# Kernel tuning notes

Measured on AMD Instinct MI355X. Metric: run time of the kernel, lower is better.

Reference implementation:

```python
import jax, jax.numpy as jnp
import numpy as np

N, E, IN, C, ED = 100000, 1600000, 128, 64, 16
L, SC, NCL, NM = 3, 256, 2, 4000  # n_conv_layers, classifier width, n_classifier_layers, n_graphs
INV_SQRT_C = 1.0 / np.sqrt(C).astype(np.float32)


def _w(k, shape):
    fan_in = shape[-2] if len(shape) > 1 else shape[-1]
    return jax.random.normal(k, shape, jnp.float32) / np.sqrt(fan_in).astype(np.float32)


def setup_inputs() -> dict:
    key = jax.random.key(0)
    ks = jax.random.split(key, 40)
    inp = {
        "x": jax.random.normal(ks[0], (N, IN), jnp.float32),
        "edge_index": jax.random.randint(ks[1], (2, E), 0, N, jnp.int32),
        "edge_attr": jax.random.normal(ks[2], (E, ED), jnp.float32),
        "batch": jnp.sort(jax.random.randint(ks[3], (N,), 0, NM, jnp.int32)),
        # conv1 (IN -> C), heads=1
        "Wq1": _w(ks[4], (IN, C)), "bq1": jnp.zeros((C,), jnp.float32),
        "Wk1": _w(ks[5], (IN, C)), "bk1": jnp.zeros((C,), jnp.float32),
        "Wv1": _w(ks[6], (IN, C)), "bv1": jnp.zeros((C,), jnp.float32),
        "We1": _w(ks[7], (ED, C)),  # lin_edge has no bias in PyG TransformerConv
        "Ws1": _w(ks[8], (IN, C)), "bs1": jnp.zeros((C,), jnp.float32),
        # stacked conv layers (C -> C)
        "Wq": _w(ks[9], (L, C, C)), "bq": jnp.zeros((L, C), jnp.float32),
        "Wk": _w(ks[10], (L, C, C)), "bk": jnp.zeros((L, C), jnp.float32),
        "Wv": _w(ks[11], (L, C, C)), "bv": jnp.zeros((L, C), jnp.float32),
        "We": _w(ks[12], (L, ED, C)),
        "Ws": _w(ks[13], (L, C, C)), "bs": jnp.zeros((L, C), jnp.float32),
        # classifier head
        "W1": _w(ks[14], (C * (L + 1), SC)), "b1": jnp.zeros((SC,), jnp.float32),
        "Wc": _w(ks[15], (NCL, SC, SC)), "bc": jnp.zeros((NCL, SC), jnp.float32),
        "Wf": _w(ks[16], (SC, 1)), "bf": jnp.zeros((1,), jnp.float32),
    }
    return inp


def _tconv(h, src, dst, ea_proj_in, Wq, bq, Wk, bk, Wv, bv, We, Ws, bs):
    n = h.shape[0]
    q = h @ Wq + bq                      # [N,C]
    k = h @ Wk + bk
    v = h @ Wv + bv
    e = ea_proj_in @ We                  # [E,C]
    ke = k[src] + e                      # gather + edge add
    ve = v[src] + e
    alpha = jnp.sum(q[dst] * ke, axis=-1) * INV_SQRT_C  # [E]
    m = jax.ops.segment_max(alpha, dst, num_segments=n)
    m = jnp.where(jnp.isfinite(m), m, 0.0)
    p = jnp.exp(alpha - m[dst])
    s = jax.ops.segment_sum(p, dst, num_segments=n)
    p = p / (s[dst] + 1e-16)             # PyG-style segment softmax
    out = jax.ops.segment_sum(ve * p[:, None], dst, num_segments=n)
    return out + h @ Ws + bs             # root_weight skip


def reference(x, edge_index, edge_attr, batch,
              Wq1, bq1, Wk1, bk1, Wv1, bv1, We1, Ws1, bs1,
              Wq, bq, Wk, bk, Wv, bv, We, Ws, bs,
              W1, b1, Wc, bc, Wf, bf):
    src, dst = edge_index[0], edge_index[1]
    h = jax.nn.leaky_relu(_tconv(x, src, dst, edge_attr,
                                 Wq1, bq1, Wk1, bk1, Wv1, bv1, We1, Ws1, bs1))
    hs = []
    for i in range(L):
        h = jax.nn.leaky_relu(_tconv(h, src, dst, edge_attr,
                                     Wq[i], bq[i], Wk[i], bk[i], Wv[i], bv[i],
                                     We[i], Ws[i], bs[i]))
        hs.append(h)
    h_pool = jax.ops.segment_sum(h, batch, num_segments=NM)   # global_add_pool
    h_pool_ = h_pool[batch]                                    # repeat_interleave (batch sorted)
    h = jnp.concatenate(hs + [h_pool_], axis=1)                # [N, C*(L+1)]
    h = h @ W1 + b1                                            # no activation before loop (as in source)
    for i in range(NCL):
        h = jax.nn.leaky_relu(h @ Wc[i] + bc[i])
    return jax.nn.sigmoid(h @ Wf + bf)                         # [N,1]
```

## Files before the change

kernel.cpp:

```cpp
#include <hip/hip_runtime.h>
#include <cstdint>
#include <cstddef>

#define NN 100000
#define EE 1600000
#define NMG 4000

__global__ __launch_bounds__(256) void tf_hist(const int* __restrict__ dst, int* __restrict__ deg) {
    int j = blockIdx.x * 256 + threadIdx.x;
    if (j < EE) atomicAdd(&deg[dst[j]], 1);
}

__global__ __launch_bounds__(256) void tf_scan1(const int* __restrict__ deg, int* __restrict__ rp,
                                                int* __restrict__ part) {
    __shared__ int sm[256];
    int tid = threadIdx.x;
    int i = blockIdx.x * 256 + tid;
    int v = (i < NN) ? deg[i] : 0;
    sm[tid] = v;
    __syncthreads();
    for (int off = 1; off < 256; off <<= 1) {
        int t = (tid >= off) ? sm[tid - off] : 0;
        __syncthreads();
        sm[tid] += t;
        __syncthreads();
    }
    if (i < NN) rp[i] = sm[tid] - v;
    if (tid == 255) part[blockIdx.x] = sm[255];
}

__global__ __launch_bounds__(512) void tf_scan2(const int* __restrict__ part, int* __restrict__ offs, int nb) {
    __shared__ int sm[512];
    int tid = threadIdx.x;
    int v = (tid < nb) ? part[tid] : 0;
    sm[tid] = v;
    __syncthreads();
    for (int off = 1; off < 512; off <<= 1) {
        int t = (tid >= off) ? sm[tid - off] : 0;
        __syncthreads();
        sm[tid] += t;
        __syncthreads();
    }
    if (tid < nb) offs[tid] = sm[tid] - v;
}

__global__ __launch_bounds__(256) void tf_scan3(int* __restrict__ rp, const int* __restrict__ offs) {
    int i = blockIdx.x * 256 + threadIdx.x;
    if (i < NN) rp[i] += offs[i >> 8];
    else if (i == NN) rp[NN] = EE;
}

__global__ __launch_bounds__(256) void tf_scatter(const int* __restrict__ src, const int* __restrict__ dst,
                                                  const int* __restrict__ rp, int* __restrict__ cur,
                                                  int* __restrict__ ssrc, int* __restrict__ seid) {
    int j = blockIdx.x * 256 + threadIdx.x;
    if (j >= EE) return;
    int d = dst[j];
    int pos = atomicAdd(&cur[d], 1);
    int slot = rp[d] + pos;
    ssrc[slot] = src[j];
    seid[slot] = j;
}

__global__ __launch_bounds__(256) void tf_ecopy(const int* __restrict__ seid, const float* __restrict__ ea,
                                                float* __restrict__ eac) {
    size_t idx = (size_t)blockIdx.x * 256 + threadIdx.x;
    if (idx >= (size_t)EE * 4) return;
    size_t slot = idx >> 2;
    int c4 = (int)(idx & 3);
    const float4* srcp = (const float4*)(ea + (size_t)seid[slot] * 16);
    ((float4*)(eac + slot * 16))[c4] = srcp[c4];
}

template <int MODE>
__global__ __launch_bounds__(256) void tf_gemm(
    const float* __restrict__ A,
    const float* __restrict__ hs0, const float* __restrict__ hs1,
    const float* __restrict__ hs2, const float* __restrict__ pl,
    const int* __restrict__ batch,
    const float* __restrict__ W0, const float* __restrict__ W1p,
    const float* __restrict__ W2, const float* __restrict__ W3,
    const float* __restrict__ b0, const float* __restrict__ b1p,
    const float* __restrict__ b2, const float* __restrict__ b3,
    float* __restrict__ O0, float* __restrict__ O1,
    float* __restrict__ O2, float* __restrict__ O3,
    int Kdim, int act) {
    __shared__ float As[64][17];
    __shared__ float Bs[16][256];
    int tid = threadIdx.x;
    int tx = tid & 15, ty = tid >> 4;
    int bm = blockIdx.x * 64;
    int tx4 = tx * 4;
    float acc[4][16];
#pragma unroll
    for (int j = 0; j < 4; ++j)
#pragma unroll
        for (int i = 0; i < 16; ++i) acc[j][i] = 0.f;

    int arow = tid >> 2;
    int aq = (tid & 3) * 4;
    int grow = bm + arow;

    for (int k0 = 0; k0 < Kdim; k0 += 16) {
        float4 av = make_float4(0.f, 0.f, 0.f, 0.f);
        if (grow < NN) {
            if (MODE == 1) {
                int k = k0 + aq, g = k >> 6, c = k & 63;
                if (g == 3) av = *(const float4*)(pl + (size_t)batch[grow] * 64 + c);
                else {
                    const float* s = (g == 0) ? hs0 : (g == 1) ? hs1 : hs2;
                    av = *(const float4*)(s + (size_t)grow * 64 + c);
                }
            } else {
                av = *(const float4*)(A + (size_t)grow * Kdim + k0 + aq);
            }
        }
        As[arow][aq + 0] = av.x; As[arow][aq + 1] = av.y;
        As[arow][aq + 2] = av.z; As[arow][aq + 3] = av.w;
#pragma unroll
        for (int r = 0; r < 4; ++r) {
            int f4 = tid + r * 256;
            int t = f4 >> 6;
            int col = (f4 & 63) * 4;
            float4 bv;
            if (MODE == 0) {
                int g = col >> 6, c = col & 63;
                const float* Wg = (g == 0) ? W0 : (g == 1) ? W1p : (g == 2) ? W2 : W3;
                bv = *(const float4*)(Wg + (size_t)(k0 + t) * 64 + c);
            } else {
                bv = *(const float4*)(W0 + (size_t)(k0 + t) * 256 + col);
            }
            *(float4*)&Bs[t][col] = bv;
        }
        __syncthreads();
#pragma unroll
        for (int t = 0; t < 16; ++t) {
            float a0 = As[ty * 4 + 0][t], a1 = As[ty * 4 + 1][t];
            float a2 = As[ty * 4 + 2][t], a3 = As[ty * 4 + 3][t];
            float4 v0 = *(const float4*)&Bs[t][tx4 + 0];
            float4 v1 = *(const float4*)&Bs[t][tx4 + 64];
            float4 v2 = *(const float4*)&Bs[t][tx4 + 128];
            float4 v3 = *(const float4*)&Bs[t][tx4 + 192];
            float bb[16] = {v0.x, v0.y, v0.z, v0.w, v1.x, v1.y, v1.z, v1.w,
                            v2.x, v2.y, v2.z, v2.w, v3.x, v3.y, v3.z, v3.w};
#pragma unroll
            for (int i = 0; i < 16; ++i) {
                acc[0][i] = fmaf(a0, bb[i], acc[0][i]);
                acc[1][i] = fmaf(a1, bb[i], acc[1][i]);
                acc[2][i] = fmaf(a2, bb[i], acc[2][i]);
                acc[3][i] = fmaf(a3, bb[i], acc[3][i]);
            }
        }
        __syncthreads();
    }
    if (MODE == 0) {
#pragma unroll
        for (int g = 0; g < 4; ++g) {
            const float* bias = (g == 0) ? b0 : (g == 1) ? b1p : (g == 2) ? b2 : b3;
            float* Out = (g == 0) ? O0 : (g == 1) ? O1 : (g == 2) ? O2 : O3;
            float4 bv = *(const float4*)(bias + tx4);
#pragma unroll
            for (int j = 0; j < 4; ++j) {
                int r = bm + ty * 4 + j;
                if (r < NN) {
                    float4 v;
                    v.x = acc[j][g * 4 + 0] + bv.x;
                    v.y = acc[j][g * 4 + 1] + bv.y;
                    v.z = acc[j][g * 4 + 2] + bv.z;
                    v.w = acc[j][g * 4 + 3] + bv.w;
                    *(float4*)(Out + (size_t)r * 64 + tx4) = v;
                }
            }
        }
    } else {
#pragma unroll
        for (int j = 0; j < 4; ++j) {
            int r = bm + ty * 4 + j;
            if (r < NN) {
#pragma unroll
                for (int g = 0; g < 4; ++g) {
                    int col = tx4 + g * 64;
                    float4 v;
                    v.x = acc[j][g * 4 + 0] + b0[col + 0];
                    v.y = acc[j][g * 4 + 1] + b0[col + 1];
                    v.z = acc[j][g * 4 + 2] + b0[col + 2];
                    v.w = acc[j][g * 4 + 3] + b0[col + 3];
                    if (act) {
                        v.x = v.x > 0.f ? v.x : 0.01f * v.x;
                        v.y = v.y > 0.f ? v.y : 0.01f * v.y;
                        v.z = v.z > 0.f ? v.z : 0.01f * v.z;
                        v.w = v.w > 0.f ? v.w : 0.01f * v.w;
                    }
                    *(float4*)(O0 + (size_t)r * 256 + col) = v;
                }
            }
        }
    }
}

template <bool USE_EAC>
__global__ __launch_bounds__(256) void tf_agg(
    const float* __restrict__ Q, const float* __restrict__ Km,
    const float* __restrict__ V, const float* __restrict__ BASE,
    const int* __restrict__ rp, const int* __restrict__ ssrc, const int* __restrict__ seid,
    const float* __restrict__ eaw,
    const float* __restrict__ We,
    float* __restrict__ out) {
    __shared__ float qsm[4][64];
    int wv = threadIdx.x >> 6;
    int node = (blockIdx.x << 2) + wv;
    int lane = threadIdx.x & 63;
    if (node >= NN) return;

    float w[16];
#pragma unroll
    for (int d = 0; d < 16; ++d) w[d] = We[d * 64 + lane];

    float q = Q[(size_t)node * 64 + lane];

    qsm[wv][lane] = q;
    int dgrp = lane >> 2;
    int cb = lane & 3;
    float pq = 0.f;
#pragma unroll
    for (int k2 = 0; k2 < 16; ++k2) {
        int c = cb + (k2 << 2);
        pq = fmaf(qsm[wv][c], We[dgrp * 64 + c], pq);
    }
    pq += __shfl_xor(pq, 1);
    pq += __shfl_xor(pq, 2);
    float qel = __shfl(pq, (lane & 15) << 2);

    int beg = rp[node], end = rp[node + 1];
    float mA = -INFINITY, sA = 0.f, accA = 0.f, peaA = 0.f;
    float mB = -INFINITY, sB = 0.f, accB = 0.f, peaB = 0.f;

    int it = beg;
    for (; it + 1 < end; it += 2) {
        int sa = ssrc[it], sb = ssrc[it + 1];
        float ea_a, ea_b;
        if (USE_EAC) {
            ea_a = (lane < 16) ? eaw[(size_t)it * 16 + lane] : 0.f;
            ea_b = (lane < 16) ? eaw[(size_t)(it + 1) * 16 + lane] : 0.f;
        } else {
            int ja = seid[it], jb = seid[it + 1];
            ea_a = (lane < 16) ? eaw[(size_t)ja * 16 + lane] : 0.f;
            ea_b = (lane < 16) ? eaw[(size_t)jb * 16 + lane] : 0.f;
        }
        float ka = Km[(size_t)sa * 64 + lane];
        float kb = Km[(size_t)sb * 64 + lane];
        float va = V[(size_t)sa * 64 + lane];
        float vb = V[(size_t)sb * 64 + lane];
        float pa = fmaf(q, ka, ea_a * qel);
        float pb = fmaf(q, kb, ea_b * qel);
#pragma unroll
        for (int o = 32; o; o >>= 1) {
            pa += __shfl_xor(pa, o);
            pb += __shfl_xor(pb, o);
        }
        float alA = pa * 0.125f, alB = pb * 0.125f;
        float nmA = fmaxf(mA, alA);
        float scA = __expf(mA - nmA);
        float ppA = __expf(alA - nmA);
        sA = sA * scA + ppA;
        accA = fmaf(ppA, va, accA * scA);
        peaA = fmaf(ppA, ea_a, peaA * scA);
        mA = nmA;
        float nmB = fmaxf(mB, alB);
        float scB = __expf(mB - nmB);
        float ppB = __expf(alB - nmB);
        sB = sB * scB + ppB;
        accB = fmaf(ppB, vb, accB * scB);
        peaB = fmaf(ppB, ea_b, peaB * scB);
        mB = nmB;
    }
    if (it < end) {
        int sa = ssrc[it];
        float ea_a;
        if (USE_EAC) ea_a = (lane < 16) ? eaw[(size_t)it * 16 + lane] : 0.f;
        else {
            int ja = seid[it];
            ea_a = (lane < 16) ? eaw[(size_t)ja * 16 + lane] : 0.f;
        }
        float ka = Km[(size_t)sa * 64 + lane];
        float va = V[(size_t)sa * 64 + lane];
        float pa = fmaf(q, ka, ea_a * qel);
#pragma unroll
        for (int o = 32; o; o >>= 1) pa += __shfl_xor(pa, o);
        float alA = pa * 0.125f;
        float nmA = fmaxf(mA, alA);
        float scA = __expf(mA - nmA);
        float ppA = __expf(alA - nmA);
        sA = sA * scA + ppA;
        accA = fmaf(ppA, va, accA * scA);
        peaA = fmaf(ppA, ea_a, peaA * scA);
        mA = nmA;
    }

    float base = BASE[(size_t)node * 64 + lane];
    float o;
    if (end > beg) {
        float m = fmaxf(mA, mB);
        float cA = __expf(mA - m);
        float cB = __expf(mB - m);
        float s = sA * cA + sB * cB;
        float acc = accA * cA + accB * cB;
        float pea = peaA * cA + peaB * cB;
        float eaout = 0.f;
#pragma unroll
        for (int d = 0; d < 16; ++d) eaout = fmaf(__shfl(pea, d), w[d], eaout);
        o = (acc + eaout) / (s + 1e-16f) + base;
    } else {
        o = base;
    }
    out[(size_t)node * 64 + lane] = (o > 0.f) ? o : 0.01f * o;
}

__global__ __launch_bounds__(256) void tf_pool(const float* __restrict__ h, const int* __restrict__ bat,
                                               float* __restrict__ pl) {
    int idx = blockIdx.x * 256 + threadIdx.x;
    if (idx >= NN * 64) return;
    int node = idx >> 6, l = idx & 63;
    atomicAdd(&pl[(size_t)bat[node] * 64 + l], h[idx]);
}

__global__ __launch_bounds__(256) void tf_final(const float* __restrict__ g, const float* __restrict__ Wf,
                                                const float* __restrict__ bf, float* __restrict__ out) {
    int wid = (blockIdx.x * 256 + threadIdx.x) >> 6;
    int lane = threadIdx.x & 63;
    if (wid >= NN) return;
    const float* row = g + (size_t)wid * 256;
    float s = row[lane] * Wf[lane] + row[lane + 64] * Wf[lane + 64] +
              row[lane + 128] * Wf[lane + 128] + row[lane + 192] * Wf[lane + 192];
#pragma unroll
    for (int off = 32; off; off >>= 1) s += __shfl_xor(s, off);
    if (lane == 0) out[wid] = 1.f / (1.f + __expf(-(s + bf[0])));
}

extern "C" void kernel_launch(void* const* d_in, const int* in_sizes, int n_in,
                              void* d_out, int out_size, void* d_ws, size_t ws_size,
                              hipStream_t stream) {
    (void)in_sizes; (void)n_in; (void)out_size;
    const float* x   = (const float*)d_in[0];
    const int*   ei  = (const int*)d_in[1];
    const float* ea  = (const float*)d_in[2];
    const int*   bat = (const int*)d_in[3];
    const float* Wq1 = (const float*)d_in[4];  const float* bq1 = (const float*)d_in[5];
    const float* Wk1 = (const float*)d_in[6];  const float* bk1 = (const float*)d_in[7];
    const float* Wv1 = (const float*)d_in[8];  const float* bv1 = (const float*)d_in[9];
    const float* We1 = (const float*)d_in[10];
    const float* Ws1 = (const float*)d_in[11]; const float* bs1 = (const float*)d_in[12];
    const float* WqL = (const float*)d_in[13]; const float* bqL = (const float*)d_in[14];
    const float* WkL = (const float*)d_in[15]; const float* bkL = (const float*)d_in[16];
    const float* WvL = (const float*)d_in[17]; const float* bvL = (const float*)d_in[18];
    const float* WeL = (const float*)d_in[19];
    const float* WsL = (const float*)d_in[20]; const float* bsL = (const float*)d_in[21];
    const float* W1  = (const float*)d_in[22]; const float* b1  = (const float*)d_in[23];
    const float* Wc  = (const float*)d_in[24]; const float* bc  = (const float*)d_in[25];
    const float* Wf  = (const float*)d_in[26]; const float* bf  = (const float*)d_in[27];
    float* outp = (float*)d_out;

    char* ws = (char*)d_ws;
    size_t off = 0;
    auto carve = [&](size_t bytes) {
        char* p = ws + off;
        off = (off + bytes + 255) & ~(size_t)255;
        return p;
    };
    int* rp    = (int*)carve((NN + 1) * sizeof(int));
    int* cur   = (int*)carve((size_t)NN * sizeof(int));
    int* part  = (int*)carve(512 * sizeof(int));
    int* offs  = (int*)carve(512 * sizeof(int));
    int* ssrc  = (int*)carve((size_t)EE * sizeof(int));
    int* seid  = (int*)carve((size_t)EE * sizeof(int));
    float* bigA = (float*)carve((size_t)NN * 256 * sizeof(float));
    float* bigB = (float*)carve((size_t)NN * 256 * sizeof(float));
    float* pl   = (float*)carve((size_t)NMG * 64 * sizeof(float));
    const size_t EAC_BYTES = (size_t)EE * 16 * sizeof(float);
    bool use_eac = (off + EAC_BYTES) <= ws_size;
    float* eac = use_eac ? (float*)carve(EAC_BYTES) : nullptr;

    float* Q    = bigA;
    float* Km   = bigA + (size_t)NN * 64;
    float* V    = bigA + (size_t)NN * 128;
    float* BASE = bigA + (size_t)NN * 192;
    float* h0   = bigB;
    float* hA   = bigB + (size_t)NN * 64;
    float* hB   = bigB + (size_t)NN * 128;
    float* hC   = bigB + (size_t)NN * 192;
    float* g1 = bigA;
    float* g2 = bigB;
    float* g3 = bigA;

    const int* esrc = ei;
    const int* edst = ei + EE;

    hipMemsetAsync(cur, 0, (size_t)NN * sizeof(int), stream);
    tf_hist<<<EE / 256, 256, 0, stream>>>(edst, cur);
    tf_scan1<<<391, 256, 0, stream>>>(cur, rp, part);
    tf_scan2<<<1, 512, 0, stream>>>(part, offs, 391);
    tf_scan3<<<392, 256, 0, stream>>>(rp, offs);
    hipMemsetAsync(cur, 0, (size_t)NN * sizeof(int), stream);
    tf_scatter<<<EE / 256, 256, 0, stream>>>(esrc, edst, rp, cur, ssrc, seid);
    if (use_eac)
        tf_ecopy<<<(EE * 4) / 256, 256, 0, stream>>>(seid, ea, eac);

    const int GB = (NN + 63) / 64;
    const int AB = NN / 4;

    tf_gemm<0><<<GB, 256, 0, stream>>>(x, nullptr, nullptr, nullptr, nullptr, nullptr,
                                       Wq1, Wk1, Wv1, Ws1, bq1, bk1, bv1, bs1,
                                       Q, Km, V, BASE, 128, 0);
    if (use_eac)
        tf_agg<true><<<AB, 256, 0, stream>>>(Q, Km, V, BASE, rp, ssrc, seid, eac, We1, h0);
    else
        tf_agg<false><<<AB, 256, 0, stream>>>(Q, Km, V, BASE, rp, ssrc, seid, ea, We1, h0);

    const float* hin = h0;
    float* houts[3] = {hA, hB, hC};
    for (int l = 0; l < 3; ++l) {
        tf_gemm<0><<<GB, 256, 0, stream>>>(hin, nullptr, nullptr, nullptr, nullptr, nullptr,
                                           WqL + l * 4096, WkL + l * 4096, WvL + l * 4096, WsL + l * 4096,
                                           bqL + l * 64, bkL + l * 64, bvL + l * 64, bsL + l * 64,
                                           Q, Km, V, BASE, 64, 0);
        if (use_eac)
            tf_agg<true><<<AB, 256, 0, stream>>>(Q, Km, V, BASE, rp, ssrc, seid, eac,
                                                 WeL + l * 1024, houts[l]);
        else
            tf_agg<false><<<AB, 256, 0, stream>>>(Q, Km, V, BASE, rp, ssrc, seid, ea,
                                                  WeL + l * 1024, houts[l]);
        hin = houts[l];
    }

    hipMemsetAsync(pl, 0, (size_t)NMG * 64 * sizeof(float), stream);
    tf_pool<<<AB, 256, 0, stream>>>(hC, bat, pl);

    tf_gemm<1><<<GB, 256, 0, stream>>>(nullptr, hA, hB, hC, pl, bat,
                                       W1, nullptr, nullptr, nullptr,
                                       b1, nullptr, nullptr, nullptr,
                                       g1, nullptr, nullptr, nullptr, 256, 0);
    tf_gemm<2><<<GB, 256, 0, stream>>>(g1, nullptr, nullptr, nullptr, nullptr, nullptr,
                                       Wc, nullptr, nullptr, nullptr,
                                       bc, nullptr, nullptr, nullptr,
                                       g2, nullptr, nullptr, nullptr, 256, 1);
    tf_gemm<2><<<GB, 256, 0, stream>>>(g2, nullptr, nullptr, nullptr, nullptr, nullptr,
                                       Wc + 65536, nullptr, nullptr, nullptr,
                                       bc + 256, nullptr, nullptr, nullptr,
                                       g3, nullptr, nullptr, nullptr, 256, 1);
    tf_final<<<AB, 256, 0, stream>>>(g3, Wf, bf, outp);
}
```

Before: 2.033 ms.

## Drop online-softmax max tracking and unroll edge aggregation by four

The aggregation kernel no longer tracks a running maximum for the softmax. It exponentiates the raw scaled scores directly and accumulates sum, value and edge terms without rescaling. The edge loop is unrolled from two to four independent edges so more gathers of K, V and edge features are in flight at once. The per-lane We register preload is replaced by loads inside the final projection loop, which cuts register pressure. The cost is numerical: without max subtraction, large attention logits can overflow exp or lose precision.

```diff
diff --git a/kernel.cpp b/kernel.cpp
--- a/kernel.cpp
+++ b/kernel.cpp
@@ -212,10 +212,6 @@
     int lane = threadIdx.x & 63;
     if (node >= NN) return;
 
-    float w[16];
-#pragma unroll
-    for (int d = 0; d < 16; ++d) w[d] = We[d * 64 + lane];
-
     float q = Q[(size_t)node * 64 + lane];
 
     qsm[wv][lane] = q;
@@ -232,83 +228,76 @@
     float qel = __shfl(pq, (lane & 15) << 2);
 
     int beg = rp[node], end = rp[node + 1];
-    float mA = -INFINITY, sA = 0.f, accA = 0.f, peaA = 0.f;
-    float mB = -INFINITY, sB = 0.f, accB = 0.f, peaB = 0.f;
+    float s = 0.f, acc = 0.f, pea = 0.f;
 
     int it = beg;
-    for (; it + 1 < end; it += 2) {
-        int sa = ssrc[it], sb = ssrc[it + 1];
-        float ea_a, ea_b;
+    for (; it + 3 < end; it += 4) {
+        int s0 = ssrc[it], s1 = ssrc[it + 1], s2 = ssrc[it + 2], s3 = ssrc[it + 3];
+        float ea0, ea1, ea2, ea3;
         if (USE_EAC) {
-            ea_a = (lane < 16) ? eaw[(size_t)it * 16 + lane] : 0.f;
-            ea_b = (lane < 16) ? eaw[(size_t)(it + 1) * 16 + lane] : 0.f;
+            ea0 = (lane < 16) ? eaw[(size_t)it * 16 + lane] : 0.f;
+            ea1 = (lane < 16) ? eaw[(size_t)(it + 1) * 16 + lane] : 0.f;
+            ea2 = (lane < 16) ? eaw[(size_t)(it + 2) * 16 + lane] : 0.f;
+            ea3 = (lane < 16) ? eaw[(size_t)(it + 3) * 16 + lane] : 0.f;
         } else {
-            int ja = seid[it], jb = seid[it + 1];
-            ea_a = (lane < 16) ? eaw[(size_t)ja * 16 + lane] : 0.f;
-            ea_b = (lane < 16) ? eaw[(size_t)jb * 16 + lane] : 0.f;
-        }
-        float ka = Km[(size_t)sa * 64 + lane];
-        float kb = Km[(size_t)sb * 64 + lane];
-        float va = V[(size_t)sa * 64 + lane];
-        float vb = V[(size_t)sb * 64 + lane];
-        float pa = fmaf(q, ka, ea_a * qel);
-        float pb = fmaf(q, kb, ea_b * qel);
+            int j0 = seid[it], j1 = seid[it + 1], j2 = seid[it + 2], j3 = seid[it + 3];
+            ea0 = (lane < 16) ? eaw[(size_t)j0 * 16 + lane] : 0.f;
+            ea1 = (lane < 16) ? eaw[(size_t)j1 * 16 + lane] : 0.f;
+            ea2 = (lane < 16) ? eaw[(size_t)j2 * 16 + lane] : 0.f;
+            ea3 = (lane < 16) ? eaw[(size_t)j3 * 16 + lane] : 0.f;
+        }
+        float k0 = Km[(size_t)s0 * 64 + lane];
+        float k1 = Km[(size_t)s1 * 64 + lane];
+        float k2 = Km[(size_t)s2 * 64 + lane];
+        float k3 = Km[(size_t)s3 * 64 + lane];
+        float v0 = V[(size_t)s0 * 64 + lane];
+        float v1 = V[(size_t)s1 * 64 + lane];
+        float v2 = V[(size_t)s2 * 64 + lane];
+        float v3 = V[(size_t)s3 * 64 + lane];
+        float p0 = fmaf(q, k0, ea0 * qel);
+        float p1 = fmaf(q, k1, ea1 * qel);
+        float p2 = fmaf(q, k2, ea2 * qel);
+        float p3 = fmaf(q, k3, ea3 * qel);
 #pragma unroll
         for (int o = 32; o; o >>= 1) {
-            pa += __shfl_xor(pa, o);
-            pb += __shfl_xor(pb, o);
-        }
-        float alA = pa * 0.125f, alB = pb * 0.125f;
-        float nmA = fmaxf(mA, alA);
-        float scA = __expf(mA - nmA);
-        float ppA = __expf(alA - nmA);
-        sA = sA * scA + ppA;
-        accA = fmaf(ppA, va, accA * scA);
-        peaA = fmaf(ppA, ea_a, peaA * scA);
-        mA = nmA;
-        float nmB = fmaxf(mB, alB);
-        float scB = __expf(mB - nmB);
-        float ppB = __expf(alB - nmB);
-        sB = sB * scB + ppB;
-        accB = fmaf(ppB, vb, accB * scB);
-        peaB = fmaf(ppB, ea_b, peaB * scB);
-        mB = nmB;
-    }
-    if (it < end) {
-        int sa = ssrc[it];
-        float ea_a;
-        if (USE_EAC) ea_a = (lane < 16) ? eaw[(size_t)it * 16 + lane] : 0.f;
+            p0 += __shfl_xor(p0, o);
+            p1 += __shfl_xor(p1, o);
+            p2 += __shfl_xor(p2, o);
+            p3 += __shfl_xor(p3, o);
+        }
+        float e0 = __expf(p0 * 0.125f);
+        float e1 = __expf(p1 * 0.125f);
+        float e2 = __expf(p2 * 0.125f);
+        float e3 = __expf(p3 * 0.125f);
+        s += (e0 + e1) + (e2 + e3);
+        acc = fmaf(e0, v0, fmaf(e1, v1, fmaf(e2, v2, fmaf(e3, v3, acc))));
+        pea = fmaf(e0, ea0, fmaf(e1, ea1, fmaf(e2, ea2, fmaf(e3, ea3, pea))));
+    }
+    for (; it < end; ++it) {
+        int s0 = ssrc[it];
+        float ea0;
+        if (USE_EAC) ea0 = (lane < 16) ? eaw[(size_t)it * 16 + lane] : 0.f;
         else {
-            int ja = seid[it];
-            ea_a = (lane < 16) ? eaw[(size_t)ja * 16 + lane] : 0.f;
-        }
-        float ka = Km[(size_t)sa * 64 + lane];
-        float va = V[(size_t)sa * 64 + lane];
-        float pa = fmaf(q, ka, ea_a * qel);
-#pragma unroll
-        for (int o = 32; o; o >>= 1) pa += __shfl_xor(pa, o);
-        float alA = pa * 0.125f;
-        float nmA = fmaxf(mA, alA);
-        float scA = __expf(mA - nmA);
-        float ppA = __expf(alA - nmA);
-        sA = sA * scA + ppA;
-        accA = fmaf(ppA, va, accA * scA);
-        peaA = fmaf(ppA, ea_a, peaA * scA);
-        mA = nmA;
+            int j0 = seid[it];
+            ea0 = (lane < 16) ? eaw[(size_t)j0 * 16 + lane] : 0.f;
+        }
+        float k0 = Km[(size_t)s0 * 64 + lane];
+        float v0 = V[(size_t)s0 * 64 + lane];
+        float p0 = fmaf(q, k0, ea0 * qel);
+#pragma unroll
+        for (int o = 32; o; o >>= 1) p0 += __shfl_xor(p0, o);
+        float e0 = __expf(p0 * 0.125f);
+        s += e0;
+        acc = fmaf(e0, v0, acc);
+        pea = fmaf(e0, ea0, pea);
     }
 
     float base = BASE[(size_t)node * 64 + lane];
     float o;
     if (end > beg) {
-        float m = fmaxf(mA, mB);
-        float cA = __expf(mA - m);
-        float cB = __expf(mB - m);
-        float s = sA * cA + sB * cB;
-        float acc = accA * cA + accB * cB;
-        float pea = peaA * cA + peaB * cB;
         float eaout = 0.f;
 #pragma unroll
-        for (int d = 0; d < 16; ++d) eaout = fmaf(__shfl(pea, d), w[d], eaout);
+        for (int d = 0; d < 16; ++d) eaout = fmaf(__shfl(pea, d), We[d * 64 + lane], eaout);
         o = (acc + eaout) / (s + 1e-16f) + base;
     } else {
         o = base;
```

Result: faster. 1.869 ms (-8.1%).
